# Kernel tuning notes

Hardware: AMD Instinct MI355X
Metric: run time of the kernel (lower is better)

Reference implementation:

```python
import jax, jax.numpy as jnp
import numpy as np

B, N, C, H = 16, 1024, 768, 12
HD = C // H
SCALE = HD ** -0.5


def setup_inputs() -> dict:
    key = jax.random.key(0)
    k1, k2, k3 = jax.random.split(key, 3)
    x = jax.random.normal(k1, (B, N, C), dtype=jnp.float32)
    W_qkv = jax.random.normal(k2, (C, 3 * C), dtype=jnp.float32) * (C ** -0.5)
    W_proj = jax.random.normal(k3, (C, C), dtype=jnp.float32) * (C ** -0.5)
    b_proj = jnp.zeros((C,), dtype=jnp.float32)
    return {"x": x, "W_qkv": W_qkv, "W_proj": W_proj, "b_proj": b_proj}


def reference(x, W_qkv, W_proj, b_proj):
    # qkv projection: [B, N, 3C] -> chunk into q, k, v
    qkv = x @ W_qkv
    q, k, v = jnp.split(qkv, 3, axis=-1)
    # reshape to [B, H, N, HD]
    q = q.reshape(B, N, H, HD).transpose(0, 2, 1, 3)
    k = k.reshape(B, N, H, HD).transpose(0, 2, 1, 3)
    v = v.reshape(B, N, H, HD).transpose(0, 2, 1, 3)
    # manual attention: scores, softmax, weighted sum
    attn = jnp.einsum("bhqd,bhkd->bhqk", q, k) * SCALE
    attn = jax.nn.softmax(attn, axis=-1)
    out = jnp.einsum("bhqk,bhkd->bhqd", attn, v)
    out = out.transpose(0, 2, 1, 3).reshape(B, N, C)
    # output projection
    return out @ W_proj + b_proj
```

## Files before the change

kernel.cpp:

```cpp
#include <hip/hip_runtime.h>

#define B_   16
#define NH   12
#define SEQ  1024
#define CD   768
#define HD_  64
#define MTOT (B_ * SEQ)
#define QSCALE 0.18033688f

typedef __attribute__((ext_vector_type(4)))  float  f32x4;
typedef __attribute__((ext_vector_type(16))) float  f32x16;
typedef __attribute__((ext_vector_type(8)))  __bf16 bf16x8;
typedef __attribute__((ext_vector_type(2)))  unsigned u32x2;

#define WAITV8 asm volatile("s_waitcnt vmcnt(8)" ::: "memory")
#define WAITV4 asm volatile("s_waitcnt vmcnt(4)" ::: "memory")
#define WAITV0 asm volatile("s_waitcnt vmcnt(0)" ::: "memory")
#define LGKM0  asm volatile("s_waitcnt lgkmcnt(0)" ::: "memory")
#define BAR    __builtin_amdgcn_s_barrier()
#define SB0    __builtin_amdgcn_sched_barrier(0)

__device__ __forceinline__ unsigned short f2bf(float f) {
  unsigned u = __float_as_uint(f);
  u = (u + 0x7FFFu + ((u >> 16) & 1u)) >> 16;
  return (unsigned short)u;
}

__device__ __forceinline__ void gload16(const void* g, void* l) {
  __builtin_amdgcn_global_load_lds(
      (const __attribute__((address_space(1))) void*)g,
      (__attribute__((address_space(3))) void*)l, 16, 0, 0);
}

__device__ __forceinline__ u32x2 pswap(unsigned x, unsigned y) {
  return __builtin_amdgcn_permlane32_swap(x, y, false, false);
}


__global__ void cvt_x_kernel(const float* __restrict__ in,
                             unsigned short* __restrict__ out, int n4) {
  int i = blockIdx.x * blockDim.x + threadIdx.x;
  if (i >= n4) return;
  float4 f = reinterpret_cast<const float4*>(in)[i];
  uint2 o;
  o.x = (unsigned)f2bf(f.x) | ((unsigned)f2bf(f.y) << 16);
  o.y = (unsigned)f2bf(f.z) | ((unsigned)f2bf(f.w) << 16);
  reinterpret_cast<uint2*>(out)[i] = o;
}

__global__ void transpose_cvt_kernel(const float* __restrict__ W,
                                     unsigned short* __restrict__ Wt,
                                     int K, int N) {
  __shared__ float tile[32][33];
  int j0 = blockIdx.x * 32, k0 = blockIdx.y * 32;
  int tx = threadIdx.x, ty = threadIdx.y;
  #pragma unroll
  for (int i = 0; i < 4; i++)
    tile[ty + 8 * i][tx] = W[(size_t)(k0 + ty + 8 * i) * N + j0 + tx];
  __syncthreads();
  #pragma unroll
  for (int i = 0; i < 4; i++)
    Wt[(size_t)(j0 + ty + 8 * i) * K + k0 + tx] = f2bf(tile[tx][ty + 8 * i]);
}


__device__ __forceinline__ bf16x8 ldsA64(const unsigned short* buf, int row, int g) {
  int byte = (row << 6) + ((g << 4) ^ (((row >> 1) & 3) << 4));
  return *reinterpret_cast<const bf16x8*>((const char*)buf + byte);
}
__device__ __forceinline__ bf16x8 lds128(const unsigned short* buf, int row, int cb) {
  int byte = (row << 7) + (cb ^ ((row & 7) << 4));
  return *reinterpret_cast<const bf16x8*>((const char*)buf + byte);
}


template <int MODE>
__global__ __launch_bounds__(256, 3)
void gemm128_kernel(const unsigned short* __restrict__ A,
                    const unsigned short* __restrict__ Bt,
                    unsigned short* __restrict__ qkvOut,
                    unsigned short* __restrict__ vtOut,
                    float* __restrict__ outF,
                    const float* __restrict__ bias) {
  constexpr int K = 768;
  __shared__ unsigned short sbuf[24576];
  unsigned short* const A0 = sbuf;
  unsigned short* const Bb0 = sbuf + 4096;
  unsigned short* const A1 = sbuf + 8192;
  unsigned short* const Bb1 = sbuf + 12288;
  unsigned short* const A2 = sbuf + 16384;
  unsigned short* const Bb2 = sbuf + 20480;

  const int tid = threadIdx.x;
  const int lane = tid & 63;
  const int wave = tid >> 6;
  const int wm = (wave >> 1) << 6;
  const int wn = (wave & 1) << 6;
  const int m0 = blockIdx.x << 7;
  const int j0 = blockIdx.y << 7;

  const int sr = tid >> 2;
  const int sc = (tid & 3) << 4;
  const int scs = sc ^ (((sr >> 1) & 3) << 4);

  f32x4 acc[4][4] = {};

  const char* const ab  = (const char*)(A  + (size_t)(m0 + sr) * K) + scs;
  const char* const ab2 = (const char*)(A  + (size_t)(m0 + sr + 64) * K) + scs;
  const char* const bb  = (const char*)(Bt + (size_t)(j0 + sr) * K) + scs;
  const char* const bb2 = (const char*)(Bt + (size_t)(j0 + sr + 64) * K) + scs;

  auto stageT = [&](int kt, unsigned short* Ad, unsigned short* Bd) {
    const int kb = kt * 64;
    gload16(ab  + kb, (char*)Ad + tid * 16);
    gload16(ab2 + kb, (char*)Ad + 4096 + tid * 16);
    gload16(bb  + kb, (char*)Bd + tid * 16);
    gload16(bb2 + kb, (char*)Bd + 4096 + tid * 16);
  };

  auto computeT = [&](const unsigned short* As, const unsigned short* Bs) {
    bf16x8 af[4], bf[4];
    const int g = lane >> 4;
    #pragma unroll
    for (int fr = 0; fr < 4; fr++) af[fr] = ldsA64(As, wm + fr * 16 + (lane & 15), g);
    #pragma unroll
    for (int fn = 0; fn < 4; fn++) bf[fn] = ldsA64(Bs, wn + fn * 16 + (lane & 15), g);
    #pragma unroll
    for (int fr = 0; fr < 4; fr++)
      #pragma unroll
      for (int fn = 0; fn < 4; fn++)
        acc[fr][fn] = __builtin_amdgcn_mfma_f32_16x16x32_bf16(af[fr], bf[fn],
                                                              acc[fr][fn], 0, 0, 0);
  };

  stageT(0, A0, Bb0);
  stageT(1, A1, Bb1);
  stageT(2, A2, Bb2);

  #pragma unroll 1
  for (int t = 0; t < 21; t += 3) {
    WAITV8; BAR; SB0;
    computeT(A0, Bb0);
    SB0; LGKM0; BAR;
    stageT(t + 3, A0, Bb0);

    WAITV8; BAR; SB0;
    computeT(A1, Bb1);
    SB0; LGKM0; BAR;
    stageT(t + 4, A1, Bb1);

    WAITV8; BAR; SB0;
    computeT(A2, Bb2);
    SB0; LGKM0; BAR;
    stageT(t + 5, A2, Bb2);
  }
  WAITV8; BAR; SB0;
  computeT(A0, Bb0);
  WAITV4; BAR; SB0;
  computeT(A1, Bb1);
  WAITV0; BAR; SB0;
  computeT(A2, Bb2);

  const int g4 = (lane >> 4) << 2;

  if (MODE == 0) {
    LGKM0; BAR;
    const bool secV = (j0 >= 1536);
    const float scale = (j0 < 768) ? QSCALE : 1.0f;
    char* const ct = (char*)sbuf;
    #pragma unroll
    for (int fr = 0; fr < 4; fr++) {
      #pragma unroll
      for (int fn = 0; fn < 4; fn++) {
        const int j_l = wn + fn * 16 + (lane & 15);
        #pragma unroll
        for (int r = 0; r < 4; r++) {
          const int m_l = wm + fr * 16 + g4 + r;
          const unsigned short v = f2bf(acc[fr][fn][r] * scale);
          const int addr = secV ? (j_l * 288 + m_l * 2) : (m_l * 288 + j_l * 2);
          *reinterpret_cast<unsigned short*>(ct + addr) = v;
        }
      }
    }
    LGKM0; BAR;
    const int c = tid & 15, r0 = tid >> 4;
    if (!secV) {
      char* const gb = (char*)qkvOut + (size_t)m0 * 4608 + j0 * 2 + c * 16;
      #pragma unroll
      for (int k = 0; k < 8; k++) {
        const int row = r0 + 16 * k;
        const uint4 d = *reinterpret_cast<const uint4*>(ct + row * 288 + c * 16);
        *reinterpret_cast<uint4*>(gb + (size_t)row * 4608) = d;
      }
    } else {
      const int b = m0 >> 10, nblk = (m0 & 1023) >> 7;
      const int h0 = (j0 - 1536) >> 6;
      char* const vb = (char*)vtOut +
          ((size_t)(b * NH + h0) * 65536 + (size_t)nblk * 8192) * 2 + c * 16;
      #pragma unroll
      for (int k = 0; k < 8; k++) {
        const int row = r0 + 16 * k;
        const uint4 d = *reinterpret_cast<const uint4*>(ct + row * 288 + c * 16);
        const size_t off = ((size_t)(row >> 6) * 65536 + (size_t)(row & 63) * 128) * 2;
        *reinterpret_cast<uint4*>(vb + off) = d;
      }
    }
  } else {
    #pragma unroll
    for (int fr = 0; fr < 4; fr++) {
      #pragma unroll
      for (int fn = 0; fn < 4; fn++) {
        const int jl = j0 + wn + fn * 16 + (lane & 15);
        const int mb = m0 + wm + fr * 16 + g4;
        const float bv = bias[jl];
        #pragma unroll
        for (int r = 0; r < 4; r++)
          outF[(size_t)(mb + r) * CD + jl] = acc[fr][fn][r] + bv;
      }
    }
  }
}


__global__ __launch_bounds__(256, 4)
void attn_kernel(const unsigned short* __restrict__ qkvB,
                 const unsigned short* __restrict__ Vt,
                 unsigned short* __restrict__ Og) {
  __shared__ unsigned short ldsbuf[16384];
  __shared__ float sStat[2][4][32];

  unsigned short* const K0 = ldsbuf;
  unsigned short* const V0 = ldsbuf + 4096;
  unsigned short* const K1 = ldsbuf + 8192;
  unsigned short* const V1 = ldsbuf + 12288;
  unsigned short* const Qs = ldsbuf + 8192;

  const int tid = threadIdx.x;
  const int lane = tid & 63;
  const int wave = tid >> 6;
  const int half = lane >> 5;
  const int q_l = lane & 31;
  const int bh = blockIdx.x;
  const int q0 = blockIdx.y * 128;
  const int b = bh / NH, head = bh - b * NH;

  const int sr = tid >> 3;
  const int scs = ((tid & 7) << 4) ^ ((sr & 7) << 4);

  const char* const xb_ = (const char*)qkvB + (size_t)b * 1024 * 4608;
  const int qoff = head * 128;
  const int koff = qoff + 1536;
  const char* const vb0 = (const char*)Vt + (size_t)bh * 131072;

  {
    #pragma unroll
    for (int i = 0; i < 4; i++)
      gload16(xb_ + (size_t)(q0 + sr + 32 * i) * 4608 + qoff + scs,
              (char*)Qs + (tid + 256 * i) * 16);
    gload16(xb_ + (size_t)sr * 4608 + koff + scs, (char*)K0 + tid * 16);
    gload16(xb_ + (size_t)(sr + 32) * 4608 + koff + scs, (char*)K0 + 4096 + tid * 16);
    gload16(vb0 + sr * 256 + scs, (char*)V0 + tid * 16);
    gload16(vb0 + (sr + 32) * 256 + scs, (char*)V0 + 4096 + tid * 16);
  }
  __syncthreads();

  bf16x8 qf[4];
  #pragma unroll
  for (int c = 0; c < 4; c++)
    qf[c] = lds128(Qs, wave * 32 + q_l, 32 * c + 16 * half);
  __syncthreads();

  f32x16 o0 = {}, o1 = {};
  float mrun = -1e30f, lrun = 0.f;

  for (int t = 0; t < 16; t++) {
    const unsigned short* const Kc = (t & 1) ? K1 : K0;
    const unsigned short* const Vc = (t & 1) ? V1 : V0;
    unsigned short* const Kn = (t & 1) ? K0 : K1;
    unsigned short* const Vn = (t & 1) ? V0 : V1;
    if (t < 15) {
      const int kv1 = (t + 1) * 64;
      const char* const vtile = vb0 + (kv1 >> 7) * 16384 + ((kv1 >> 6) & 1) * 128;
      gload16(xb_ + (size_t)(kv1 + sr) * 4608 + koff + scs, (char*)Kn + tid * 16);
      gload16(xb_ + (size_t)(kv1 + sr + 32) * 4608 + koff + scs,
              (char*)Kn + 4096 + tid * 16);
      gload16(vtile + sr * 256 + scs, (char*)Vn + tid * 16);
      gload16(vtile + (sr + 32) * 256 + scs, (char*)Vn + 4096 + tid * 16);
    }

    f32x16 s0 = {}, s1 = {};
    #pragma unroll
    for (int c = 0; c < 4; c++) {
      bf16x8 kf0 = lds128(Kc, q_l, 32 * c + 16 * half);
      bf16x8 kf1 = lds128(Kc, 32 + q_l, 32 * c + 16 * half);
      s0 = __builtin_amdgcn_mfma_f32_32x32x16_bf16(kf0, qf[c], s0, 0, 0, 0);
      s1 = __builtin_amdgcn_mfma_f32_32x32x16_bf16(kf1, qf[c], s1, 0, 0, 0);
    }

    float vmax = fmaxf(s0[0], s1[0]);
    #pragma unroll
    for (int r = 1; r < 16; r++) vmax = fmaxf(vmax, fmaxf(s0[r], s1[r]));
    {
      u32x2 mx = pswap(__float_as_uint(vmax), __float_as_uint(vmax));
      vmax = fmaxf(__uint_as_float(mx[0]), __uint_as_float(mx[1]));
    }

    if (!__all(vmax <= mrun + 8.0f)) {
      const float mnew = fmaxf(mrun, vmax);
      const float corr = __builtin_amdgcn_exp2f(mrun - mnew);
      mrun = mnew;
      lrun *= corr;
      if (lane < 32) sStat[0][wave][q_l] = corr;
      f32x4 c4[4];
      #pragma unroll
      for (int j = 0; j < 4; j++)
        c4[j] = *reinterpret_cast<const f32x4*>(&sStat[0][wave][4 * half + 8 * j]);
      #pragma unroll
      for (int r = 0; r < 16; r++) {
        const float cc = c4[r >> 2][r & 3];
        o0[r] *= cc;
        o1[r] *= cc;
      }
    }

    float tsum = 0.f;
    #pragma unroll
    for (int r = 0; r < 16; r++) {
      const float p0 = __builtin_amdgcn_exp2f(s0[r] - mrun);
      const float p1 = __builtin_amdgcn_exp2f(s1[r] - mrun);
      s0[r] = p0; s1[r] = p1;
      tsum += p0 + p1;
    }
    {
      u32x2 ts = pswap(__float_as_uint(tsum), __float_as_uint(tsum));
      tsum = __uint_as_float(ts[0]) + __uint_as_float(ts[1]);
    }
    lrun += tsum;

    unsigned pk[2][8];
    #pragma unroll
    for (int w = 0; w < 8; w++) {
      asm("v_cvt_pk_bf16_f32 %0, %1, %2"
          : "=v"(pk[0][w]) : "v"(s0[2 * w]), "v"(s0[2 * w + 1]));
      asm("v_cvt_pk_bf16_f32 %0, %1, %2"
          : "=v"(pk[1][w]) : "v"(s1[2 * w]), "v"(s1[2 * w + 1]));
    }

    #pragma unroll
    for (int c = 0; c < 4; c++) {
      const int st = c >> 1, cc = c & 1;
      u32x2 rA = pswap(pk[st][4 * cc + 0], pk[st][4 * cc + 2]);
      u32x2 rB = pswap(pk[st][4 * cc + 1], pk[st][4 * cc + 3]);
      union { unsigned u[4]; bf16x8 v; } pa;
      pa.u[0] = rA[0]; pa.u[1] = rB[0]; pa.u[2] = rA[1]; pa.u[3] = rB[1];
      bf16x8 vf0 = lds128(Vc, q_l, 32 * c + 16 * half);
      bf16x8 vf1 = lds128(Vc, 32 + q_l, 32 * c + 16 * half);
      o0 = __builtin_amdgcn_mfma_f32_32x32x16_bf16(pa.v, vf0, o0, 0, 0, 0);
      o1 = __builtin_amdgcn_mfma_f32_32x32x16_bf16(pa.v, vf1, o1, 0, 0, 0);
    }
    __syncthreads();
  }

  if (lane < 32) sStat[1][wave][q_l] = lrun;
  f32x4 rl4[4];
  #pragma unroll
  for (int j = 0; j < 4; j++) {
    f32x4 lv = *reinterpret_cast<const f32x4*>(&sStat[1][wave][4 * half + 8 * j]);
    #pragma unroll
    for (int e = 0; e < 4; e++) rl4[j][e] = __builtin_amdgcn_rcpf(lv[e]);
  }
  #pragma unroll
  for (int r = 0; r < 16; r++) {
    const int qq = q0 + wave * 32 + (r & 3) + 8 * (r >> 2) + 4 * half;
    const float rl = rl4[r >> 2][r & 3];
    const size_t base = ((size_t)b * SEQ + qq) * CD + head * HD_;
    Og[base + q_l]      = f2bf(o0[r] * rl);
    Og[base + 32 + q_l] = f2bf(o1[r] * rl);
  }
}


extern "C" void kernel_launch(void* const* d_in, const int* in_sizes, int n_in,
                              void* d_out, int out_size, void* d_ws, size_t ws_size,
                              hipStream_t stream) {
  const float* x     = (const float*)d_in[0];
  const float* Wqkv  = (const float*)d_in[1];
  const float* Wproj = (const float*)d_in[2];
  const float* bproj = (const float*)d_in[3];

  char* ws = (char*)d_ws;
  unsigned short* qkvB = (unsigned short*)(ws + 0);
  unsigned short* Vt   = (unsigned short*)(ws + 75497472);
  unsigned short* xb   = (unsigned short*)(ws + 100663296);
  unsigned short* ao   = (unsigned short*)(ws + 100663296);
  unsigned short* wqT  = (unsigned short*)(ws + 125829120);
  unsigned short* wpT  = (unsigned short*)(ws + 129368064);
  if (ws_size < 130547712ull) return;

  const int n4 = MTOT * CD / 4;
  cvt_x_kernel<<<n4 / 256, 256, 0, stream>>>(x, xb, n4);
  transpose_cvt_kernel<<<dim3(2304 / 32, 768 / 32), dim3(32, 8), 0, stream>>>(Wqkv, wqT, 768, 2304);
  transpose_cvt_kernel<<<dim3(768 / 32, 768 / 32), dim3(32, 8), 0, stream>>>(Wproj, wpT, 768, 768);

  gemm128_kernel<0><<<dim3(128, 18), 256, 0, stream>>>(xb, wqT, qkvB, Vt,
                                                       nullptr, nullptr);
  attn_kernel<<<dim3(B_ * NH, SEQ / 128), 256, 0, stream>>>(qkvB, Vt, ao);
  gemm128_kernel<1><<<dim3(128, 6), 256, 0, stream>>>(ao, wpT, nullptr, nullptr,
                                                      (float*)d_out, bproj);
}
```

Baseline: 197.6 us.

## Merge prep kernels into one launch and restructure GEMM pipeline to one barrier per stage

Fuses the x conversion and both weight transpose-convert kernels into a single prep kernel, removing two launches. Restructures the triple-buffered GEMM main loop so each stage issues the next global-to-LDS load before computing, with one barrier per stage instead of two and a prefetch depth of two. Also raises wave priority around the MFMA block. The reduced prefetch depth and barrier removal change how load latency is hidden, which could expose memory stalls.

```diff
diff --git a/kernel.cpp b/kernel.cpp
--- a/kernel.cpp
+++ b/kernel.cpp
@@ -13,12 +13,11 @@
 typedef __attribute__((ext_vector_type(8)))  __bf16 bf16x8;
 typedef __attribute__((ext_vector_type(2)))  unsigned u32x2;
 
-#define WAITV8 asm volatile("s_waitcnt vmcnt(8)" ::: "memory")
-#define WAITV4 asm volatile("s_waitcnt vmcnt(4)" ::: "memory")
-#define WAITV0 asm volatile("s_waitcnt vmcnt(0)" ::: "memory")
-#define LGKM0  asm volatile("s_waitcnt lgkmcnt(0)" ::: "memory")
-#define BAR    __builtin_amdgcn_s_barrier()
-#define SB0    __builtin_amdgcn_sched_barrier(0)
+#define WAITV4  asm volatile("s_waitcnt vmcnt(4)" ::: "memory")
+#define WAITV0  asm volatile("s_waitcnt vmcnt(0)" ::: "memory")
+#define LGKM0   asm volatile("s_waitcnt lgkmcnt(0)" ::: "memory")
+#define BAR     __builtin_amdgcn_s_barrier()
+#define SB0     __builtin_amdgcn_sched_barrier(0)
 
 __device__ __forceinline__ unsigned short f2bf(float f) {
   unsigned u = __float_as_uint(f);
@@ -37,30 +36,40 @@
 }
 
 
-__global__ void cvt_x_kernel(const float* __restrict__ in,
-                             unsigned short* __restrict__ out, int n4) {
-  int i = blockIdx.x * blockDim.x + threadIdx.x;
-  if (i >= n4) return;
-  float4 f = reinterpret_cast<const float4*>(in)[i];
-  uint2 o;
-  o.x = (unsigned)f2bf(f.x) | ((unsigned)f2bf(f.y) << 16);
-  o.y = (unsigned)f2bf(f.z) | ((unsigned)f2bf(f.w) << 16);
-  reinterpret_cast<uint2*>(out)[i] = o;
-}
-
-__global__ void transpose_cvt_kernel(const float* __restrict__ W,
-                                     unsigned short* __restrict__ Wt,
-                                     int K, int N) {
+__global__ __launch_bounds__(256)
+void prep_kernel(const float* __restrict__ x,
+                 const float* __restrict__ Wqkv,
+                 const float* __restrict__ Wproj,
+                 unsigned short* __restrict__ xb,
+                 unsigned short* __restrict__ wqT,
+                 unsigned short* __restrict__ wpT) {
   __shared__ float tile[32][33];
-  int j0 = blockIdx.x * 32, k0 = blockIdx.y * 32;
-  int tx = threadIdx.x, ty = threadIdx.y;
-  #pragma unroll
-  for (int i = 0; i < 4; i++)
-    tile[ty + 8 * i][tx] = W[(size_t)(k0 + ty + 8 * i) * N + j0 + tx];
-  __syncthreads();
-  #pragma unroll
-  for (int i = 0; i < 4; i++)
-    Wt[(size_t)(j0 + ty + 8 * i) * K + k0 + tx] = f2bf(tile[tx][ty + 8 * i]);
+  const int bid = blockIdx.x;
+  const int tid = threadIdx.x;
+  if (bid < 12288) {
+    const int i = bid * 256 + tid;
+    float4 f = reinterpret_cast<const float4*>(x)[i];
+    uint2 o;
+    o.x = (unsigned)f2bf(f.x) | ((unsigned)f2bf(f.y) << 16);
+    o.y = (unsigned)f2bf(f.z) | ((unsigned)f2bf(f.w) << 16);
+    reinterpret_cast<uint2*>(xb)[i] = o;
+  } else {
+    const float* W;
+    unsigned short* Wt;
+    int N, b2;
+    if (bid < 12288 + 1728) { b2 = bid - 12288; W = Wqkv; Wt = wqT; N = 2304; }
+    else                    { b2 = bid - 14016; W = Wproj; Wt = wpT; N = 768; }
+    const int nb = N / 32;
+    const int j0 = (b2 % nb) * 32, k0 = (b2 / nb) * 32;
+    const int tx = tid & 31, ty = tid >> 5;
+    #pragma unroll
+    for (int i = 0; i < 4; i++)
+      tile[ty + 8 * i][tx] = W[(size_t)(k0 + ty + 8 * i) * N + j0 + tx];
+    __syncthreads();
+    #pragma unroll
+    for (int i = 0; i < 4; i++)
+      Wt[(size_t)(j0 + ty + 8 * i) * 768 + k0 + tx] = f2bf(tile[tx][ty + 8 * i]);
+  }
 }
 
 
@@ -125,36 +134,35 @@
     for (int fr = 0; fr < 4; fr++) af[fr] = ldsA64(As, wm + fr * 16 + (lane & 15), g);
     #pragma unroll
     for (int fn = 0; fn < 4; fn++) bf[fn] = ldsA64(Bs, wn + fn * 16 + (lane & 15), g);
+    __builtin_amdgcn_s_setprio(1);
     #pragma unroll
     for (int fr = 0; fr < 4; fr++)
       #pragma unroll
       for (int fn = 0; fn < 4; fn++)
         acc[fr][fn] = __builtin_amdgcn_mfma_f32_16x16x32_bf16(af[fr], bf[fn],
                                                               acc[fr][fn], 0, 0, 0);
+    __builtin_amdgcn_s_setprio(0);
   };
 
   stageT(0, A0, Bb0);
   stageT(1, A1, Bb1);
-  stageT(2, A2, Bb2);
 
   #pragma unroll 1
   for (int t = 0; t < 21; t += 3) {
-    WAITV8; BAR; SB0;
+    WAITV4; BAR; SB0;
+    stageT(t + 2, A2, Bb2);
     computeT(A0, Bb0);
-    SB0; LGKM0; BAR;
+
+    WAITV4; BAR; SB0;
     stageT(t + 3, A0, Bb0);
-
-    WAITV8; BAR; SB0;
     computeT(A1, Bb1);
-    SB0; LGKM0; BAR;
+
+    WAITV4; BAR; SB0;
     stageT(t + 4, A1, Bb1);
-
-    WAITV8; BAR; SB0;
     computeT(A2, Bb2);
-    SB0; LGKM0; BAR;
-    stageT(t + 5, A2, Bb2);
-  }
-  WAITV8; BAR; SB0;
+  }
+  WAITV4; BAR; SB0;
+  stageT(23, A2, Bb2);
   computeT(A0, Bb0);
   WAITV4; BAR; SB0;
   computeT(A1, Bb1);
@@ -173,11 +181,12 @@
       #pragma unroll
       for (int fn = 0; fn < 4; fn++) {
         const int j_l = wn + fn * 16 + (lane & 15);
+        const int m_l = wm + fr * 16 + g4;
         #pragma unroll
         for (int r = 0; r < 4; r++) {
-          const int m_l = wm + fr * 16 + g4 + r;
           const unsigned short v = f2bf(acc[fr][fn][r] * scale);
-          const int addr = secV ? (j_l * 288 + m_l * 2) : (m_l * 288 + j_l * 2);
+          const int addr = secV ? (j_l * 288 + (m_l + r) * 2)
+                                : ((m_l + r) * 288 + j_l * 2);
           *reinterpret_cast<unsigned short*>(ct + addr) = v;
         }
       }
@@ -397,11 +406,7 @@
   unsigned short* wpT  = (unsigned short*)(ws + 129368064);
   if (ws_size < 130547712ull) return;
 
-  const int n4 = MTOT * CD / 4;
-  cvt_x_kernel<<<n4 / 256, 256, 0, stream>>>(x, xb, n4);
-  transpose_cvt_kernel<<<dim3(2304 / 32, 768 / 32), dim3(32, 8), 0, stream>>>(Wqkv, wqT, 768, 2304);
-  transpose_cvt_kernel<<<dim3(768 / 32, 768 / 32), dim3(32, 8), 0, stream>>>(Wproj, wpT, 768, 768);
-
+  prep_kernel<<<14592, 256, 0, stream>>>(x, Wqkv, Wproj, xb, wqT, wpT);
   gemm128_kernel<0><<<dim3(128, 18), 256, 0, stream>>>(xb, wqT, qkvB, Vt,
                                                        nullptr, nullptr);
   attn_kernel<<<dim3(B_ * NH, SEQ / 128), 256, 0, stream>>>(qkvB, Vt, ao);
```

Result: no change. 195.3 us (-1.2%).
